# Kernel optimization log

Measured on AMD Instinct MI355X. Metric: run time of the kernel, lower is better.

Reference implementation:

```python
import jax, jax.numpy as jnp
import numpy as np

CORR_THRESHOLD = 0.3
EPS = 1e-8


def setup_inputs() -> dict:
    key = jax.random.key(0)
    x = jax.random.normal(key, (128, 8192, 64), dtype=jnp.float32)  # [B, W, D]
    return {"x": x}


def reference(x) -> jnp.ndarray:
    # x: [B, W, D]. Per-batch Pearson correlation matrix via one batched GEMM
    # (mathematically equal to the per-feature zero-lag FFT cross-correlation
    # loop in the original forward, fused into bwi,bwj).
    B, W, D = x.shape
    centered = x - jnp.mean(x, axis=1, keepdims=True)            # [B, W, D]
    cov = jnp.einsum('bwi,bwj->bij', centered, centered) / (W - 1)  # [B, D, D]
    std = jnp.sqrt(jnp.diagonal(cov, axis1=1, axis2=2)) + EPS    # [B, D] (unbiased std, matches torch.std)
    corr = cov / (std[:, :, None] * std[:, None, :])             # [B, D, D]
    significant = (jnp.abs(corr) > CORR_THRESHOLD).astype(x.dtype)
    # self-correlation is always 1 > threshold, so subtract 1
    return jnp.sum(significant, axis=2) - 1.0                    # [B, D]
```

## Files before the change

### kernel.cpp

```cpp
#include <hip/hip_runtime.h>
#include <stdint.h>

#define BATCH 128
#define W_LEN 8192
#define D_FEAT 64
#define WC 128
#define LDS_STRIDE 68
#define WS_PER_SLICE 4160

typedef __bf16 bf16x8 __attribute__((ext_vector_type(8)));
typedef float f32x4 __attribute__((ext_vector_type(4)));

union FragU { uint4 u; bf16x8 v; };

__device__ __forceinline__ unsigned int f2bf_pair(float lo, float hi) {
  unsigned int a = __float_as_uint(lo);
  unsigned int b = __float_as_uint(hi);
  a = (a + 0x7fffu + ((a >> 16) & 1u)) >> 16;
  b = (b + 0x7fffu + ((b >> 16) & 1u)) >> 16;
  return (a & 0xffffu) | (b << 16);
}

__global__ void __launch_bounds__(256)
cov_partial_kernel(const float* __restrict__ x, float* __restrict__ ws, int S) {
  __shared__ __align__(16) unsigned int lds_u[D_FEAT * LDS_STRIDE];
  __shared__ float ssum_scratch[256 * 4];
  const int tid  = threadIdx.x;
  const int lane = tid & 63;
  const int wid  = tid >> 6;
  const int s = blockIdx.x;
  const int b = blockIdx.y;
  const int ws_per   = W_LEN / S;
  const int nchunks  = ws_per / WC;

  const int q    = tid & 15;
  const int prow = tid >> 4;
  const int m    = lane & 15;
  const int hi   = lane >> 4;
  const int koff = wid * 16 + hi * 4;

  f32x4 acc[4][4];
  #pragma unroll
  for (int i = 0; i < 4; i++)
    #pragma unroll
    for (int j = 0; j < 4; j++)
      #pragma unroll
      for (int r = 0; r < 4; r++) acc[i][j][r] = 0.0f;

  float ssum[4] = {0.f, 0.f, 0.f, 0.f};

  const size_t base_row = (size_t)b * W_LEN + (size_t)s * ws_per;

  for (int c = 0; c < nchunks; c++) {
    __syncthreads();
    #pragma unroll
    for (int it = 0; it < 4; it++) {
      const int p = it * 16 + prow;
      const float* src = x + (base_row + (size_t)c * WC + 2 * p) * D_FEAT + q * 4;
      float4 fa = *(const float4*)(src);
      float4 fb = *(const float4*)(src + D_FEAT);
      ssum[0] += fa.x + fb.x;
      ssum[1] += fa.y + fb.y;
      ssum[2] += fa.z + fb.z;
      ssum[3] += fa.w + fb.w;
      lds_u[(q * 4 + 0) * LDS_STRIDE + p] = f2bf_pair(fa.x, fb.x);
      lds_u[(q * 4 + 1) * LDS_STRIDE + p] = f2bf_pair(fa.y, fb.y);
      lds_u[(q * 4 + 2) * LDS_STRIDE + p] = f2bf_pair(fa.z, fb.z);
      lds_u[(q * 4 + 3) * LDS_STRIDE + p] = f2bf_pair(fa.w, fb.w);
    }
    __syncthreads();
    FragU f[4];
    #pragma unroll
    for (int g = 0; g < 4; g++)
      f[g].u = *(const uint4*)&lds_u[(g * 16 + m) * LDS_STRIDE + koff];
    #pragma unroll
    for (int i = 0; i < 4; i++)
      #pragma unroll
      for (int j = 0; j < 4; j++)
        acc[i][j] = __builtin_amdgcn_mfma_f32_16x16x32_bf16(f[i].v, f[j].v, acc[i][j], 0, 0, 0);
  }

  __syncthreads();
  float* cov_lds = (float*)lds_u;
  for (int wv = 0; wv < 4; wv++) {
    if (wid == wv) {
      #pragma unroll
      for (int i = 0; i < 4; i++)
        #pragma unroll
        for (int j = 0; j < 4; j++)
          #pragma unroll
          for (int r = 0; r < 4; r++) {
            const int row = i * 16 + hi * 4 + r;
            const int col = j * 16 + m;
            const int idx = row * D_FEAT + col;
            if (wv == 0) cov_lds[idx] = acc[i][j][r];
            else         cov_lds[idx] += acc[i][j][r];
          }
    }
    __syncthreads();
  }

  #pragma unroll
  for (int j = 0; j < 4; j++) ssum_scratch[tid * 4 + j] = ssum[j];
  __syncthreads();

  float* out_base = ws + (size_t)(b * S + s) * WS_PER_SLICE;
  if (tid < D_FEAT) {
    const int qq = tid >> 2, jj = tid & 3;
    float t = 0.f;
    #pragma unroll
    for (int g = 0; g < 16; g++) t += ssum_scratch[(g * 16 + qq) * 4 + jj];
    out_base[4096 + tid] = t;
  }
  #pragma unroll
  for (int it = 0; it < 4; it++) {
    const int idx = (it * 256 + tid) * 4;
    *(float4*)&out_base[idx] = *(const float4*)&cov_lds[idx];
  }
}

__global__ void __launch_bounds__(256)
corr_count_kernel(const float* __restrict__ ws, float* __restrict__ out, int S) {
  __shared__ __align__(16) float cov[4096];
  __shared__ float sums[D_FEAT];
  __shared__ float rstd[D_FEAT];
  __shared__ float cnts[256];
  const int tid = threadIdx.x;
  const int b = blockIdx.x;
  const float* base = ws + (size_t)b * S * WS_PER_SLICE;

  #pragma unroll
  for (int it = 0; it < 4; it++) {
    const int idx = (it * 256 + tid) * 4;
    float ax = 0.f, ay = 0.f, az = 0.f, aw = 0.f;
    for (int s = 0; s < S; s++) {
      float4 v = *(const float4*)&base[(size_t)s * WS_PER_SLICE + idx];
      ax += v.x; ay += v.y; az += v.z; aw += v.w;
    }
    float4 a; a.x = ax; a.y = ay; a.z = az; a.w = aw;
    *(float4*)&cov[idx] = a;
  }
  if (tid < D_FEAT) {
    float t = 0.f;
    for (int s = 0; s < S; s++) t += base[(size_t)s * WS_PER_SLICE + 4096 + tid];
    sums[tid] = t;
  }
  __syncthreads();
  if (tid < D_FEAT) {
    const float sd = sums[tid];
    float c = (cov[tid * D_FEAT + tid] - sd * sd * (1.0f / W_LEN)) * (1.0f / (W_LEN - 1));
    c = c > 0.f ? c : 0.f;
    rstd[tid] = 1.0f / (sqrtf(c) + 1e-8f);
  }
  __syncthreads();
  {
    const int r = tid >> 2, part = tid & 3;
    const float sr = sums[r];
    const float rs_r = rstd[r];
    float cnt = 0.f;
    #pragma unroll
    for (int k = 0; k < 16; k++) {
      const int cc = part * 16 + k;
      const float cv = (cov[r * D_FEAT + cc] - sr * sums[cc] * (1.0f / W_LEN)) * (1.0f / (W_LEN - 1));
      const float corr = cv * rs_r * rstd[cc];
      cnt += (fabsf(corr) > 0.3f) ? 1.0f : 0.0f;
    }
    cnts[tid] = cnt;
  }
  __syncthreads();
  if (tid < D_FEAT) {
    const float t = cnts[tid * 4] + cnts[tid * 4 + 1] + cnts[tid * 4 + 2] + cnts[tid * 4 + 3];
    out[(size_t)b * D_FEAT + tid] = t - 1.0f;
  }
}

extern "C" void kernel_launch(void* const* d_in, const int* in_sizes, int n_in,
                              void* d_out, int out_size, void* d_ws, size_t ws_size,
                              hipStream_t stream) {
  const float* x = (const float*)d_in[0];
  float* out = (float*)d_out;
  float* ws  = (float*)d_ws;

  int S = 8;
  while (S > 1 && (size_t)BATCH * S * WS_PER_SLICE * sizeof(float) > ws_size) S >>= 1;

  dim3 g1(S, BATCH);
  cov_partial_kernel<<<g1, 256, 0, stream>>>(x, ws, S);
  corr_count_kernel<<<BATCH, 256, 0, stream>>>(ws, out, S);
}
```

Measured before the change: 373.0 us.

## Double-buffer LDS, prefetch next chunk, split output tiles across waves

Loads for the next chunk are issued into registers before the MFMA phase, and a double-buffered LDS lets one barrier per chunk replace two. Each wave now owns a 16-row block of the 64x64 output and loops over the whole K range, rather than owning a K slice of the full output. This removes the serial cross-wave LDS reduction and lets results go straight to global memory. It also swaps round-to-nearest bf16 conversion for truncation via a byte permute, which gives up some accuracy, and adds a launch-bounds occupancy hint.

```diff
diff --git a/kernel.cpp b/kernel.cpp
--- a/kernel.cpp
+++ b/kernel.cpp
@@ -6,6 +6,7 @@
 #define D_FEAT 64
 #define WC 128
 #define LDS_STRIDE 68
+#define LDSU (D_FEAT * LDS_STRIDE)
 #define WS_PER_SLICE 4160
 
 typedef __bf16 bf16x8 __attribute__((ext_vector_type(8)));
@@ -13,109 +14,95 @@
 
 union FragU { uint4 u; bf16x8 v; };
 
-__device__ __forceinline__ unsigned int f2bf_pair(float lo, float hi) {
-  unsigned int a = __float_as_uint(lo);
-  unsigned int b = __float_as_uint(hi);
-  a = (a + 0x7fffu + ((a >> 16) & 1u)) >> 16;
-  b = (b + 0x7fffu + ((b >> 16) & 1u)) >> 16;
-  return (a & 0xffffu) | (b << 16);
+__device__ __forceinline__ unsigned int pack_bf16_pair(float a, float b) {
+  return __builtin_amdgcn_perm(__float_as_uint(b), __float_as_uint(a), 0x07060302u);
 }
 
-__global__ void __launch_bounds__(256)
+__global__ void __launch_bounds__(256, 4)
 cov_partial_kernel(const float* __restrict__ x, float* __restrict__ ws, int S) {
-  __shared__ __align__(16) unsigned int lds_u[D_FEAT * LDS_STRIDE];
+  __shared__ __align__(16) unsigned int lds_u[2][LDSU];
   __shared__ float ssum_scratch[256 * 4];
   const int tid  = threadIdx.x;
   const int lane = tid & 63;
   const int wid  = tid >> 6;
   const int s = blockIdx.x;
   const int b = blockIdx.y;
-  const int ws_per   = W_LEN / S;
-  const int nchunks  = ws_per / WC;
+  const int ws_per  = W_LEN / S;
+  const int nchunks = ws_per / WC;
 
-  const int q    = tid & 15;
-  const int prow = tid >> 4;
-  const int m    = lane & 15;
-  const int hi   = lane >> 4;
-  const int koff = wid * 16 + hi * 4;
+  const int q = tid & 15;
+  const int T = tid >> 4;
+  const int m  = lane & 15;
+  const int hi = lane >> 4;
 
-  f32x4 acc[4][4];
+  f32x4 acc[4];
   #pragma unroll
-  for (int i = 0; i < 4; i++)
+  for (int t = 0; t < 4; t++)
     #pragma unroll
-    for (int j = 0; j < 4; j++)
-      #pragma unroll
-      for (int r = 0; r < 4; r++) acc[i][j][r] = 0.0f;
+    for (int r = 0; r < 4; r++) acc[t][r] = 0.0f;
 
   float ssum[4] = {0.f, 0.f, 0.f, 0.f};
 
-  const size_t base_row = (size_t)b * W_LEN + (size_t)s * ws_per;
+  const size_t base = ((size_t)b * W_LEN + (size_t)s * ws_per) * D_FEAT;
+  const float* src0 = x + base + (size_t)(8 * T) * D_FEAT + 4 * q;
+
+  float4 ld[8];
+  #pragma unroll
+  for (int r = 0; r < 8; r++) ld[r] = *(const float4*)(src0 + r * D_FEAT);
 
   for (int c = 0; c < nchunks; c++) {
+    unsigned int* buf = lds_u[c & 1];
+    #pragma unroll
+    for (int j = 0; j < 4; j++) {
+      const float* f0 = (const float*)&ld[0];
+      uint4 pk;
+      pk.x = pack_bf16_pair(f0[0 * 4 + j], f0[1 * 4 + j]);
+      pk.y = pack_bf16_pair(f0[2 * 4 + j], f0[3 * 4 + j]);
+      pk.z = pack_bf16_pair(f0[4 * 4 + j], f0[5 * 4 + j]);
+      pk.w = pack_bf16_pair(f0[6 * 4 + j], f0[7 * 4 + j]);
+      ssum[j] += ((f0[0 * 4 + j] + f0[1 * 4 + j]) + (f0[2 * 4 + j] + f0[3 * 4 + j]))
+               + ((f0[4 * 4 + j] + f0[5 * 4 + j]) + (f0[6 * 4 + j] + f0[7 * 4 + j]));
+      *(uint4*)&buf[(4 * q + j) * LDS_STRIDE + 4 * T] = pk;
+    }
+    if (c + 1 < nchunks) {
+      const float* srcn = src0 + (size_t)(c + 1) * WC * D_FEAT;
+      #pragma unroll
+      for (int r = 0; r < 8; r++) ld[r] = *(const float4*)(srcn + r * D_FEAT);
+    }
     __syncthreads();
     #pragma unroll
-    for (int it = 0; it < 4; it++) {
-      const int p = it * 16 + prow;
-      const float* src = x + (base_row + (size_t)c * WC + 2 * p) * D_FEAT + q * 4;
-      float4 fa = *(const float4*)(src);
-      float4 fb = *(const float4*)(src + D_FEAT);
-      ssum[0] += fa.x + fb.x;
-      ssum[1] += fa.y + fb.y;
-      ssum[2] += fa.z + fb.z;
-      ssum[3] += fa.w + fb.w;
-      lds_u[(q * 4 + 0) * LDS_STRIDE + p] = f2bf_pair(fa.x, fb.x);
-      lds_u[(q * 4 + 1) * LDS_STRIDE + p] = f2bf_pair(fa.y, fb.y);
-      lds_u[(q * 4 + 2) * LDS_STRIDE + p] = f2bf_pair(fa.z, fb.z);
-      lds_u[(q * 4 + 3) * LDS_STRIDE + p] = f2bf_pair(fa.w, fb.w);
+    for (int st = 0; st < 4; st++) {
+      const int ko = st * 16 + hi * 4;
+      FragU fA;
+      fA.u = *(const uint4*)&buf[(16 * wid + m) * LDS_STRIDE + ko];
+      #pragma unroll
+      for (int t = 0; t < 4; t++) {
+        FragU fB;
+        fB.u = *(const uint4*)&buf[(16 * t + m) * LDS_STRIDE + ko];
+        acc[t] = __builtin_amdgcn_mfma_f32_16x16x32_bf16(fA.v, fB.v, acc[t], 0, 0, 0);
+      }
     }
-    __syncthreads();
-    FragU f[4];
-    #pragma unroll
-    for (int g = 0; g < 4; g++)
-      f[g].u = *(const uint4*)&lds_u[(g * 16 + m) * LDS_STRIDE + koff];
-    #pragma unroll
-    for (int i = 0; i < 4; i++)
-      #pragma unroll
-      for (int j = 0; j < 4; j++)
-        acc[i][j] = __builtin_amdgcn_mfma_f32_16x16x32_bf16(f[i].v, f[j].v, acc[i][j], 0, 0, 0);
   }
 
-  __syncthreads();
-  float* cov_lds = (float*)lds_u;
-  for (int wv = 0; wv < 4; wv++) {
-    if (wid == wv) {
-      #pragma unroll
-      for (int i = 0; i < 4; i++)
-        #pragma unroll
-        for (int j = 0; j < 4; j++)
-          #pragma unroll
-          for (int r = 0; r < 4; r++) {
-            const int row = i * 16 + hi * 4 + r;
-            const int col = j * 16 + m;
-            const int idx = row * D_FEAT + col;
-            if (wv == 0) cov_lds[idx] = acc[i][j][r];
-            else         cov_lds[idx] += acc[i][j][r];
-          }
+  float* out_base = ws + (size_t)(b * S + s) * WS_PER_SLICE;
+  #pragma unroll
+  for (int t = 0; t < 4; t++)
+    #pragma unroll
+    for (int r = 0; r < 4; r++) {
+      const int row = 16 * wid + hi * 4 + r;
+      const int col = 16 * t + m;
+      out_base[row * D_FEAT + col] = acc[t][r];
     }
-    __syncthreads();
-  }
 
   #pragma unroll
   for (int j = 0; j < 4; j++) ssum_scratch[tid * 4 + j] = ssum[j];
   __syncthreads();
-
-  float* out_base = ws + (size_t)(b * S + s) * WS_PER_SLICE;
   if (tid < D_FEAT) {
     const int qq = tid >> 2, jj = tid & 3;
     float t = 0.f;
     #pragma unroll
     for (int g = 0; g < 16; g++) t += ssum_scratch[(g * 16 + qq) * 4 + jj];
     out_base[4096 + tid] = t;
-  }
-  #pragma unroll
-  for (int it = 0; it < 4; it++) {
-    const int idx = (it * 256 + tid) * 4;
-    *(float4*)&out_base[idx] = *(const float4*)&cov_lds[idx];
   }
 }
 
```

Result: no change. 366.6 us (-1.7%).
